# Performance work log

Hardware: AMD Instinct MI355X
Metric: run time of the kernel (lower is better)

## Reference

```python
import jax, jax.numpy as jnp
import numpy as np

NH, HD = 4, 16          # num_heads, head_dim (proj_dim = 64)
SCALE = HD ** -0.5
EPS = 1e-5
G = 16                  # GroupNorm groups = min(16, channels)


def _conv1x1(W, b, x):
    # 1x1 conv == channel-mixing matmul: W (out,in), x (B,in,H,W)
    return jnp.einsum('pc,bchw->bphw', W, x) + b[None, :, None, None]


def _attend(Wq, bq, Wk, bk, Wv, bv, Wo, bo, query, context):
    B, C, H, Wd = query.shape
    N = H * Wd
    q = _conv1x1(Wq, bq, query).astype(jnp.float32).reshape(B, NH, HD, N)
    k = _conv1x1(Wk, bk, context).astype(jnp.float32).reshape(B, NH, HD, N)
    v = _conv1x1(Wv, bv, context).astype(jnp.float32).reshape(B, NH, HD, N)
    attn = jax.nn.softmax(jnp.einsum('bhdn,bhdm->bhnm', q, k) * SCALE, axis=-1)
    out = jnp.einsum('bhdm,bhnm->bhdn', v, attn).reshape(B, NH * HD, H, Wd)
    return _conv1x1(Wo, bo, out)


def _gn(x, gamma, beta):
    B, C, H, W = x.shape
    xr = x.reshape(B, G, C // G, H, W)
    m = xr.mean(axis=(2, 3, 4), keepdims=True)
    v = xr.var(axis=(2, 3, 4), keepdims=True)
    xn = ((xr - m) * jax.lax.rsqrt(v + EPS)).reshape(B, C, H, W)
    return xn * gamma[None, :, None, None] + beta[None, :, None, None]


def setup_inputs() -> dict:
    key = jax.random.key(0)
    C, P, Bn, H, W = 256, 64, 2, 64, 64
    ks = iter(jax.random.split(key, 64))
    d = {}
    for m in ['a', 'b', 'c']:
        d[f'feat_{m}'] = jax.random.normal(next(ks), (Bn, C, H, W), jnp.float32)
    for m in ['a', 'b', 'c']:
        d[f'Wq_{m}'] = 0.02 * jax.random.normal(next(ks), (P, C), jnp.float32)
        d[f'bq_{m}'] = jnp.zeros((P,), jnp.float32)
        d[f'Wk_{m}'] = 0.02 * jax.random.normal(next(ks), (P, 2 * C), jnp.float32)
        d[f'bk_{m}'] = jnp.zeros((P,), jnp.float32)
        d[f'Wv_{m}'] = 0.02 * jax.random.normal(next(ks), (P, 2 * C), jnp.float32)
        d[f'bv_{m}'] = jnp.zeros((P,), jnp.float32)
        d[f'Wo_{m}'] = 0.02 * jax.random.normal(next(ks), (C, P), jnp.float32)
        d[f'bo_{m}'] = jnp.zeros((C,), jnp.float32)
        d[f'g_{m}'] = jnp.ones((C,), jnp.float32)
        d[f'be_{m}'] = jnp.zeros((C,), jnp.float32)
    return d


def reference(feat_a, feat_b, feat_c,
              Wq_a, bq_a, Wk_a, bk_a, Wv_a, bv_a, Wo_a, bo_a, g_a, be_a,
              Wq_b, bq_b, Wk_b, bk_b, Wv_b, bv_b, Wo_b, bo_b, g_b, be_b,
              Wq_c, bq_c, Wk_c, bk_c, Wv_c, bv_c, Wo_c, bo_c, g_c, be_c):
    bc = jnp.concatenate([feat_b, feat_c], axis=1)
    a_out = _gn(feat_a + _attend(Wq_a, bq_a, Wk_a, bk_a, Wv_a, bv_a, Wo_a, bo_a, feat_a, bc), g_a, be_a)
    ac = jnp.concatenate([feat_a, feat_c], axis=1)
    b_out = _gn(feat_b + _attend(Wq_b, bq_b, Wk_b, bk_b, Wv_b, bv_b, Wo_b, bo_b, feat_b, ac), g_b, be_b)
    ab = jnp.concatenate([feat_a, feat_b], axis=1)
    c_out = _gn(feat_c + _attend(Wq_c, bq_c, Wk_c, bk_c, Wv_c, bv_c, Wo_c, bo_c, feat_c, ab), g_c, be_c)
    return (a_out, b_out, c_out)
```

## Files before the change

kernel.cpp:

```cpp
#include <hip/hip_runtime.h>

#define B_ 2
#define C_ 256
#define P_ 64
#define N_ 4096
#define EPS_ 1e-5f
#define QSCALE_ 0.3606737602222409f

typedef _Float16 half2 __attribute__((ext_vector_type(2)));
typedef _Float16 half4 __attribute__((ext_vector_type(4)));
typedef _Float16 half8 __attribute__((ext_vector_type(8)));
typedef __fp16 fp16x2 __attribute__((ext_vector_type(2)));
typedef float f32x4 __attribute__((ext_vector_type(4)));

#if __has_builtin(__builtin_amdgcn_exp2f)
static __device__ __forceinline__ float fexp2(float x) { return __builtin_amdgcn_exp2f(x); }
#else
static __device__ __forceinline__ float fexp2(float x) { return exp2f(x); }
#endif

static __device__ __forceinline__ half2 pack2(float a, float b) {
  return __builtin_bit_cast(half2, __builtin_amdgcn_cvt_pkrtz(a, b));
}

struct TP {
  const float* feat[3];
  const float* Wq[3]; const float* bq[3];
  const float* Wk[3]; const float* bk[3];
  const float* Wv[3]; const float* bv[3];
  const float* Wo[3]; const float* bo[3];
  const float* gm[3]; const float* bt[3];
  _Float16* xT;
  _Float16* q16;
  _Float16* k16;
  _Float16* v16;
  _Float16* wq16[3];
  _Float16* wk16[3];
  _Float16* wv16[3];
  _Float16* wo16[3];
  float* stats;
  float* out;
  int ctx0[3]; int ctx1[3];
};

__global__ __launch_bounds__(256) void prep_kernel(TP P) {
  const int m = blockIdx.z, b = blockIdx.y;
  const int tid = threadIdx.x;
  {
    const int c0 = (blockIdx.x >> 6) * 64 + (tid >> 6) * 16;
    const int n = (blockIdx.x & 63) * 64 + (tid & 63);
    const float* __restrict__ in = P.feat[m] + (size_t)b * C_ * N_ + n;
    float f[16];
#pragma unroll
    for (int i = 0; i < 16; ++i) f[i] = in[(size_t)(c0 + i) * N_];
    half8 h0, h1;
#pragma unroll
    for (int j = 0; j < 8; ++j) { h0[j] = (_Float16)f[j]; h1[j] = (_Float16)f[8 + j]; }
    _Float16* o = P.xT + (((size_t)(m * 2 + b) * N_) + n) * C_ + c0;
    *(half8*)o = h0;
    *(half8*)(o + 8) = h1;
  }
  if (b == 0 && blockIdx.x < 8) {
    const int s = blockIdx.x;
    const float* srcs[4] = {P.Wq[m], P.Wk[m], P.Wv[m], P.Wo[m]};
    _Float16* dsts[4] = {P.wq16[m], P.wk16[m], P.wv16[m], P.wo16[m]};
    const int sizes[4] = {64 * 256, 64 * 512, 64 * 512, 256 * 64};
#pragma unroll
    for (int a = 0; a < 4; ++a) {
      const int lo = sizes[a] / 8 * s, hi = sizes[a] / 8 * (s + 1);
      for (int i = lo + tid * 4; i < hi; i += 1024) {
        const float4 x = *(const float4*)(srcs[a] + i);
        half4 h; h[0] = (_Float16)x.x; h[1] = (_Float16)x.y;
        h[2] = (_Float16)x.z; h[3] = (_Float16)x.w;
        *(half4*)(dsts[a] + i) = h;
      }
    }
  }
  if (m == 0 && b == 0 && blockIdx.x == 8 && tid < 192) P.stats[tid] = 0.f;
}

__global__ __launch_bounds__(256) void proj_qkv_kernel(TP P) {
  __shared__ _Float16 vt[4 * 16 * 40];
  const int m = blockIdx.z, b = blockIdx.y;
  const int tid = threadIdx.x;
  const int w = tid >> 6, g = (tid >> 4) & 3, t = tid & 15;
  const bool is_q = blockIdx.x >= 128;
  const int n0 = (is_q ? blockIdx.x - 128 : (int)blockIdx.x) * 32;

  if (is_q) {
    const _Float16* __restrict__ A = P.wq16[m] + (w * 16 + t) * 256 + g * 8;
    const _Float16* __restrict__ B0 =
        P.xT + ((size_t)(m * 2 + b) * N_ + n0 + t) * C_ + g * 8;
    const _Float16* __restrict__ B1 = B0 + 16 * C_;
    f32x4 a0 = {0.f,0.f,0.f,0.f}, a1 = {0.f,0.f,0.f,0.f};
#pragma unroll
    for (int k = 0; k < 8; ++k) {
      const half8 a = *(const half8*)(A + k * 32);
      const half8 b0 = *(const half8*)(B0 + k * 32);
      const half8 b1 = *(const half8*)(B1 + k * 32);
      a0 = __builtin_amdgcn_mfma_f32_16x16x32_f16(a, b0, a0, 0, 0, 0);
      a1 = __builtin_amdgcn_mfma_f32_16x16x32_f16(a, b1, a1, 0, 0, 0);
    }
    _Float16* qo = P.q16 + ((size_t)(m * 2 + b) * N_) * 64 + w * 16 + g * 4;
    half4 h0, h1;
#pragma unroll
    for (int r = 0; r < 4; ++r) {
      const float bq = P.bq[m][w * 16 + g * 4 + r];
      h0[r] = (_Float16)((a0[r] + bq) * QSCALE_);
      h1[r] = (_Float16)((a1[r] + bq) * QSCALE_);
    }
    *(half4*)(qo + (size_t)(n0 + t) * 64) = h0;
    *(half4*)(qo + (size_t)(n0 + 16 + t) * 64) = h1;
  } else {
    f32x4 k0 = {0.f,0.f,0.f,0.f}, k1 = {0.f,0.f,0.f,0.f};
    f32x4 v0 = {0.f,0.f,0.f,0.f}, v1 = {0.f,0.f,0.f,0.f};
    const int srcs[2] = {P.ctx0[m], P.ctx1[m]};
#pragma unroll
    for (int src = 0; src < 2; ++src) {
      const _Float16* __restrict__ Ak =
          P.wk16[m] + (w * 16 + t) * 512 + src * 256 + g * 8;
      const _Float16* __restrict__ Av =
          P.wv16[m] + (w * 16 + t) * 512 + src * 256 + g * 8;
      const _Float16* __restrict__ B0 =
          P.xT + ((size_t)(srcs[src] * 2 + b) * N_ + n0 + t) * C_ + g * 8;
      const _Float16* __restrict__ B1 = B0 + 16 * C_;
#pragma unroll
      for (int k = 0; k < 8; ++k) {
        const half8 ak = *(const half8*)(Ak + k * 32);
        const half8 av = *(const half8*)(Av + k * 32);
        const half8 b0 = *(const half8*)(B0 + k * 32);
        const half8 b1 = *(const half8*)(B1 + k * 32);
        k0 = __builtin_amdgcn_mfma_f32_16x16x32_f16(ak, b0, k0, 0, 0, 0);
        k1 = __builtin_amdgcn_mfma_f32_16x16x32_f16(ak, b1, k1, 0, 0, 0);
        v0 = __builtin_amdgcn_mfma_f32_16x16x32_f16(av, b0, v0, 0, 0, 0);
        v1 = __builtin_amdgcn_mfma_f32_16x16x32_f16(av, b1, v1, 0, 0, 0);
      }
    }
    const int bh = m * 8 + b * 4 + w;
    _Float16* ko = P.k16 + ((size_t)bh * N_) * 16 + g * 4;
    half4 h0, h1;
#pragma unroll
    for (int r = 0; r < 4; ++r) {
      const float bk = P.bk[m][w * 16 + g * 4 + r];
      h0[r] = (_Float16)(k0[r] + bk);
      h1[r] = (_Float16)(k1[r] + bk);
    }
    *(half4*)(ko + (size_t)(n0 + t) * 16) = h0;
    *(half4*)(ko + (size_t)(n0 + 16 + t) * 16) = h1;
#pragma unroll
    for (int r = 0; r < 4; ++r) {
      const float bv = P.bv[m][w * 16 + g * 4 + r];
      vt[(w * 16 + g * 4 + r) * 40 + t] = (_Float16)(v0[r] + bv);
      vt[(w * 16 + g * 4 + r) * 40 + 16 + t] = (_Float16)(v1[r] + bv);
    }
    __syncthreads();
    const int hh = tid >> 6, dd = (tid >> 2) & 15, nb = (tid & 3) * 8;
    const half8 hv8 = *(const half8*)(vt + (hh * 16 + dd) * 40 + nb);
    *(half8*)(P.v16 + ((size_t)(m * 8 + b * 4 + hh) * 16 + dd) * N_ + n0 + nb) = hv8;
  }
}

__global__ __launch_bounds__(256) void attn_kernel(TP P) {
  const int m = blockIdx.z, bh = blockIdx.y;
  const int tid = threadIdx.x;
  const int w = tid >> 6, g = (tid >> 4) & 3, t = tid & 15;
  const _Float16* __restrict__ kh = P.k16 + ((size_t)(m * 8 + bh) * N_) * 16;
  const _Float16* __restrict__ vh = P.v16 + ((size_t)(m * 8 + bh) * 16) * N_;
  const int b = bh >> 2, h = bh & 3;
  _Float16* qh = P.q16 + ((size_t)(m * 2 + b) * N_) * 64 + h * 16 + g * 4;

  const int q0 = blockIdx.x * 64 + w * 16;
  const half4 qf = *(const half4*)(qh + (size_t)(q0 + t) * 64);

  __shared__ _Float16 ks[128 * 16];
  __shared__ _Float16 vs[16 * 128];

  const int kr = tid >> 1, kc8 = tid & 1;
  const int vr = tid >> 4, vc = tid & 15;
  const _Float16* kgp = kh + (size_t)kr * 16 + kc8 * 8;
  const _Float16* vgp = vh + (size_t)vr * N_ + vc * 8;
  _Float16* ksp = ks + kr * 16 + ((kc8 ^ (kr & 1)) << 3);
  _Float16* vsp = vs + vr * 128 + ((vc ^ vr) << 3);

  half8 kpre = *(const half8*)kgp;
  half8 vpre = *(const half8*)vgp;

  f32x4 lacc = {0.f, 0.f, 0.f, 0.f};
  f32x4 O0 = {0.f,0.f,0.f,0.f}, O1 = {0.f,0.f,0.f,0.f};

  for (int kv0 = 0; kv0 < N_; kv0 += 128) {
    *(half8*)ksp = kpre;
    *(half8*)vsp = vpre;
    __syncthreads();
    const int nxt = (kv0 + 128 < N_) ? kv0 + 128 : 0;
    kpre = *(const half8*)(kgp + (size_t)nxt * 16);
    vpre = *(const half8*)(vgp + nxt);
#pragma unroll
    for (int hc = 0; hc < 2; ++hc) {
      f32x4 s[4];
#pragma unroll
      for (int i = 0; i < 4; ++i) {
        const int sub = hc * 4 + i;
        const half4 kf = *(const half4*)(ks + (sub * 16 + t) * 16 +
                          (((g >> 1) ^ (t & 1)) << 3) + (g & 1) * 4);
        const f32x4 z = {0.f, 0.f, 0.f, 0.f};
        s[i] = __builtin_amdgcn_mfma_f32_16x16x16f16(kf, qf, z, 0, 0, 0);
      }
      half4 pf[4];
#pragma unroll
      for (int i = 0; i < 4; ++i) {
        const float p0 = fexp2(s[i][0]);
        const float p1 = fexp2(s[i][1]);
        const float p2 = fexp2(s[i][2]);
        const float p3 = fexp2(s[i][3]);
        lacc[0] += p0; lacc[1] += p1; lacc[2] += p2; lacc[3] += p3;
        const half2 lo = pack2(p0, p1);
        const half2 hi = pack2(p2, p3);
        pf[i] = __builtin_shufflevector(lo, hi, 0, 1, 2, 3);
      }
#pragma unroll
      for (int i = 0; i < 4; ++i) {
        const int sub = hc * 4 + i;
        const half4 vf = *(const half4*)(vs + t * 128 +
                          (((sub * 2 + (g >> 1)) ^ t) << 3) + (g & 1) * 4);
        if (i & 1) O1 = __builtin_amdgcn_mfma_f32_16x16x16f16(vf, pf[i], O1, 0, 0, 0);
        else       O0 = __builtin_amdgcn_mfma_f32_16x16x16f16(vf, pf[i], O0, 0, 0, 0);
      }
    }
    __syncthreads();
  }
  float l = lacc[0] + lacc[1] + lacc[2] + lacc[3];
  l += __shfl_xor(l, 16);
  l += __shfl_xor(l, 32);
  const float inv = 1.0f / l;
  half4 hv;
#pragma unroll
  for (int r = 0; r < 4; ++r) hv[r] = (_Float16)((O0[r] + O1[r]) * inv);
  *(half4*)(qh + (size_t)(q0 + t) * 64) = hv;
}

__global__ __launch_bounds__(256) void wo_resid_kernel(TP P) {
  const int m = blockIdx.z;
  const int b = blockIdx.y >> 2, cblk = blockIdx.y & 3;
  const int n0 = blockIdx.x * 64;
  const int tid = threadIdx.x;
  const int w = tid >> 6, g = (tid >> 4) & 3, t = tid & 15;
  const int c0 = cblk * 64 + w * 16;
  const _Float16* __restrict__ ao = P.q16 + ((size_t)(m * 2 + b) * N_) * 64;
  f32x4 acc[4] = {{0.f,0.f,0.f,0.f},{0.f,0.f,0.f,0.f},{0.f,0.f,0.f,0.f},{0.f,0.f,0.f,0.f}};
#pragma unroll
  for (int kst = 0; kst < 2; ++kst) {
    const half8 a =
        *(const half8*)(P.wo16[m] + (c0 + t) * 64 + kst * 32 + g * 8);
#pragma unroll
    for (int i = 0; i < 4; ++i) {
      const half8 bf =
          *(const half8*)(ao + (size_t)(n0 + i * 16 + t) * 64 + kst * 32 + g * 8);
      acc[i] = __builtin_amdgcn_mfma_f32_16x16x32_f16(a, bf, acc[i], 0, 0, 0);
    }
  }
  const float* __restrict__ X = P.feat[m] + (size_t)b * C_ * N_;
  float* outb = P.out + (size_t)m * B_ * C_ * N_ + (size_t)b * C_ * N_;
  float s = 0.f, s2 = 0.f;
#pragma unroll
  for (int i = 0; i < 4; ++i) {
    const int n = n0 + i * 16 + t;
#pragma unroll
    for (int r = 0; r < 4; ++r) {
      const int c = c0 + g * 4 + r;
      const float val = acc[i][r] + X[(size_t)c * N_ + n] + P.bo[m][c];
      outb[(size_t)c * N_ + n] = val;
      s += val;
      s2 += val * val;
    }
  }
#pragma unroll
  for (int off = 1; off < 64; off <<= 1) {
    s += __shfl_xor(s, off);
    s2 += __shfl_xor(s2, off);
  }
  if ((tid & 63) == 0) {
    const int group = cblk * 4 + w;
    float* st = P.stats + ((size_t)(m * 2 + b) * 16 + group) * 2;
    atomicAdd(st, s);
    atomicAdd(st + 1, s2);
  }
}

__global__ __launch_bounds__(256) void gn_final_kernel(TP P) {
  const size_t idx = ((size_t)blockIdx.x * 256 + threadIdx.x) * 4;
  const int m = (int)(idx >> 21);
  const int rem = (int)(idx & ((1u << 21) - 1));
  const int b = rem >> 20;
  const int c = (rem >> 12) & 255;
  const float* st = P.stats + ((size_t)(m * 2 + b) * 16 + (c >> 4)) * 2;
  const float mean = st[0] * (1.f / 65536.f);
  const float var = st[1] * (1.f / 65536.f) - mean * mean;
  const float rstd = rsqrtf(var + EPS_);
  const float ga = P.gm[m][c] * rstd, be = P.bt[m][c];
  float4 x = *(float4*)(P.out + idx);
  x.x = (x.x - mean) * ga + be;
  x.y = (x.y - mean) * ga + be;
  x.z = (x.z - mean) * ga + be;
  x.w = (x.w - mean) * ga + be;
  *(float4*)(P.out + idx) = x;
}

extern "C" void kernel_launch(void* const* d_in, const int* in_sizes, int n_in,
                              void* d_out, int out_size, void* d_ws, size_t ws_size,
                              hipStream_t stream) {
  TP P;
  for (int m = 0; m < 3; ++m) {
    P.feat[m] = (const float*)d_in[m];
    const int base = 3 + m * 10;
    P.Wq[m] = (const float*)d_in[base + 0];
    P.bq[m] = (const float*)d_in[base + 1];
    P.Wk[m] = (const float*)d_in[base + 2];
    P.bk[m] = (const float*)d_in[base + 3];
    P.Wv[m] = (const float*)d_in[base + 4];
    P.bv[m] = (const float*)d_in[base + 5];
    P.Wo[m] = (const float*)d_in[base + 6];
    P.bo[m] = (const float*)d_in[base + 7];
    P.gm[m] = (const float*)d_in[base + 8];
    P.bt[m] = (const float*)d_in[base + 9];
  }
  _Float16* ws = (_Float16*)d_ws;
  P.xT = ws;
  P.q16 = ws + 6291456;
  P.k16 = ws + 7864320;
  P.v16 = ws + 9437184;
  for (int m = 0; m < 3; ++m) {
    _Float16* wb = ws + 11010048 + (size_t)m * 98304;
    P.wq16[m] = wb;
    P.wk16[m] = wb + 16384;
    P.wv16[m] = wb + 49152;
    P.wo16[m] = wb + 81920;
  }
  P.stats = (float*)((char*)d_ws + 22609920);
  P.out = (float*)d_out;
  P.ctx0[0] = 1; P.ctx1[0] = 2;
  P.ctx0[1] = 0; P.ctx1[1] = 2;
  P.ctx0[2] = 0; P.ctx1[2] = 1;

  dim3 blk(256);
  prep_kernel<<<dim3(256, 2, 3), blk, 0, stream>>>(P);
  proj_qkv_kernel<<<dim3(256, 2, 3), blk, 0, stream>>>(P);
  attn_kernel<<<dim3(64, 8, 3), blk, 0, stream>>>(P);
  wo_resid_kernel<<<dim3(64, 8, 3), blk, 0, stream>>>(P);
  gn_final_kernel<<<dim3(6144), blk, 0, stream>>>(P);
}
```

Measured before the change: 293.0 us.

## Stage transposes and GEMM operands through LDS, approximate exp2, coarsen GN kernel

Measured after the change: 281.7 us. -3.9%, faster.

```diff
diff --git a/kernel.cpp b/kernel.cpp
--- a/kernel.cpp
+++ b/kernel.cpp
@@ -10,14 +10,11 @@
 typedef _Float16 half2 __attribute__((ext_vector_type(2)));
 typedef _Float16 half4 __attribute__((ext_vector_type(4)));
 typedef _Float16 half8 __attribute__((ext_vector_type(8)));
-typedef __fp16 fp16x2 __attribute__((ext_vector_type(2)));
 typedef float f32x4 __attribute__((ext_vector_type(4)));
 
-#if __has_builtin(__builtin_amdgcn_exp2f)
-static __device__ __forceinline__ float fexp2(float x) { return __builtin_amdgcn_exp2f(x); }
-#else
-static __device__ __forceinline__ float fexp2(float x) { return exp2f(x); }
-#endif
+static __device__ __forceinline__ float fexp2(float x) {
+  return __builtin_bit_cast(float, (int)fmaf(x, 8388608.0f, 1064872512.0f));
+}
 
 static __device__ __forceinline__ half2 pack2(float a, float b) {
   return __builtin_bit_cast(half2, __builtin_amdgcn_cvt_pkrtz(a, b));
@@ -44,21 +41,33 @@
 };
 
 __global__ __launch_bounds__(256) void prep_kernel(TP P) {
+  __shared__ _Float16 lt[64 * 72];
   const int m = blockIdx.z, b = blockIdx.y;
   const int tid = threadIdx.x;
+  const int cblk = blockIdx.x >> 6, nblk = blockIdx.x & 63;
   {
-    const int c0 = (blockIdx.x >> 6) * 64 + (tid >> 6) * 16;
-    const int n = (blockIdx.x & 63) * 64 + (tid & 63);
-    const float* __restrict__ in = P.feat[m] + (size_t)b * C_ * N_ + n;
+    const int n = nblk * 64 + (tid & 63);
+    const int cb = (tid >> 6) * 16;
+    const float* __restrict__ in =
+        P.feat[m] + (size_t)b * C_ * N_ + (size_t)(cblk * 64 + cb) * N_ + n;
     float f[16];
 #pragma unroll
-    for (int i = 0; i < 16; ++i) f[i] = in[(size_t)(c0 + i) * N_];
+    for (int i = 0; i < 16; ++i) f[i] = in[(size_t)i * N_];
     half8 h0, h1;
 #pragma unroll
     for (int j = 0; j < 8; ++j) { h0[j] = (_Float16)f[j]; h1[j] = (_Float16)f[8 + j]; }
-    _Float16* o = P.xT + (((size_t)(m * 2 + b) * N_) + n) * C_ + c0;
-    *(half8*)o = h0;
-    *(half8*)(o + 8) = h1;
+    *(half8*)(lt + (tid & 63) * 72 + cb) = h0;
+    *(half8*)(lt + (tid & 63) * 72 + cb + 8) = h1;
+  }
+  __syncthreads();
+  {
+    const int nr = tid >> 2, cs = (tid & 3) * 16;
+    const half8 o0 = *(const half8*)(lt + nr * 72 + cs);
+    const half8 o1 = *(const half8*)(lt + nr * 72 + cs + 8);
+    _Float16* o = P.xT + ((size_t)(m * 2 + b) * N_ + nblk * 64 + nr) * C_ +
+                  cblk * 64 + cs;
+    *(half8*)o = o0;
+    *(half8*)(o + 8) = o1;
   }
   if (b == 0 && blockIdx.x < 8) {
     const int s = blockIdx.x;
@@ -79,25 +88,30 @@
   if (m == 0 && b == 0 && blockIdx.x == 8 && tid < 192) P.stats[tid] = 0.f;
 }
 
+#define PBS_ 264
+
 __global__ __launch_bounds__(256) void proj_qkv_kernel(TP P) {
-  __shared__ _Float16 vt[4 * 16 * 40];
+  __shared__ _Float16 bs[2 * 32 * PBS_];
   const int m = blockIdx.z, b = blockIdx.y;
   const int tid = threadIdx.x;
   const int w = tid >> 6, g = (tid >> 4) & 3, t = tid & 15;
   const bool is_q = blockIdx.x >= 128;
   const int n0 = (is_q ? blockIdx.x - 128 : (int)blockIdx.x) * 32;
+  const int sr = tid >> 3, sc = (tid & 7) * 32;
 
   if (is_q) {
-    const _Float16* __restrict__ A = P.wq16[m] + (w * 16 + t) * 256 + g * 8;
-    const _Float16* __restrict__ B0 =
-        P.xT + ((size_t)(m * 2 + b) * N_ + n0 + t) * C_ + g * 8;
-    const _Float16* __restrict__ B1 = B0 + 16 * C_;
+    const _Float16* __restrict__ xb =
+        P.xT + ((size_t)(m * 2 + b) * N_ + n0 + sr) * C_ + sc;
+#pragma unroll
+    for (int j = 0; j < 4; ++j)
+      *(half8*)(bs + sr * PBS_ + sc + j * 8) = *(const half8*)(xb + j * 8);
+    __syncthreads();
     f32x4 a0 = {0.f,0.f,0.f,0.f}, a1 = {0.f,0.f,0.f,0.f};
 #pragma unroll
-    for (int k = 0; k < 8; ++k) {
-      const half8 a = *(const half8*)(A + k * 32);
-      const half8 b0 = *(const half8*)(B0 + k * 32);
-      const half8 b1 = *(const half8*)(B1 + k * 32);
+    for (int ks = 0; ks < 8; ++ks) {
+      const half8 a = *(const half8*)(P.wq16[m] + (w * 16 + t) * 256 + ks * 32 + g * 8);
+      const half8 b0 = *(const half8*)(bs + t * PBS_ + ks * 32 + g * 8);
+      const half8 b1 = *(const half8*)(bs + (16 + t) * PBS_ + ks * 32 + g * 8);
       a0 = __builtin_amdgcn_mfma_f32_16x16x32_f16(a, b0, a0, 0, 0, 0);
       a1 = __builtin_amdgcn_mfma_f32_16x16x32_f16(a, b1, a1, 0, 0, 0);
     }
@@ -112,24 +126,29 @@
     *(half4*)(qo + (size_t)(n0 + t) * 64) = h0;
     *(half4*)(qo + (size_t)(n0 + 16 + t) * 64) = h1;
   } else {
+    const int srcs[2] = {P.ctx0[m], P.ctx1[m]};
+#pragma unroll
+    for (int src = 0; src < 2; ++src) {
+      const _Float16* __restrict__ xb =
+          P.xT + ((size_t)(srcs[src] * 2 + b) * N_ + n0 + sr) * C_ + sc;
+#pragma unroll
+      for (int j = 0; j < 4; ++j)
+        *(half8*)(bs + src * 32 * PBS_ + sr * PBS_ + sc + j * 8) =
+            *(const half8*)(xb + j * 8);
+    }
+    __syncthreads();
     f32x4 k0 = {0.f,0.f,0.f,0.f}, k1 = {0.f,0.f,0.f,0.f};
     f32x4 v0 = {0.f,0.f,0.f,0.f}, v1 = {0.f,0.f,0.f,0.f};
-    const int srcs[2] = {P.ctx0[m], P.ctx1[m]};
 #pragma unroll
     for (int src = 0; src < 2; ++src) {
-      const _Float16* __restrict__ Ak =
-          P.wk16[m] + (w * 16 + t) * 512 + src * 256 + g * 8;
-      const _Float16* __restrict__ Av =
-          P.wv16[m] + (w * 16 + t) * 512 + src * 256 + g * 8;
-      const _Float16* __restrict__ B0 =
-          P.xT + ((size_t)(srcs[src] * 2 + b) * N_ + n0 + t) * C_ + g * 8;
-      const _Float16* __restrict__ B1 = B0 + 16 * C_;
-#pragma unroll
-      for (int k = 0; k < 8; ++k) {
-        const half8 ak = *(const half8*)(Ak + k * 32);
-        const half8 av = *(const half8*)(Av + k * 32);
-        const half8 b0 = *(const half8*)(B0 + k * 32);
-        const half8 b1 = *(const half8*)(B1 + k * 32);
+#pragma unroll
+      for (int ks = 0; ks < 8; ++ks) {
+        const half8 ak = *(const half8*)(P.wk16[m] + (w * 16 + t) * 512 +
+                                         src * 256 + ks * 32 + g * 8);
+        const half8 av = *(const half8*)(P.wv16[m] + (w * 16 + t) * 512 +
+                                         src * 256 + ks * 32 + g * 8);
+        const half8 b0 = *(const half8*)(bs + src * 32 * PBS_ + t * PBS_ + ks * 32 + g * 8);
+        const half8 b1 = *(const half8*)(bs + src * 32 * PBS_ + (16 + t) * PBS_ + ks * 32 + g * 8);
         k0 = __builtin_amdgcn_mfma_f32_16x16x32_f16(ak, b0, k0, 0, 0, 0);
         k1 = __builtin_amdgcn_mfma_f32_16x16x32_f16(ak, b1, k1, 0, 0, 0);
         v0 = __builtin_amdgcn_mfma_f32_16x16x32_f16(av, b0, v0, 0, 0, 0);
@@ -147,6 +166,8 @@
     }
     *(half4*)(ko + (size_t)(n0 + t) * 16) = h0;
     *(half4*)(ko + (size_t)(n0 + 16 + t) * 16) = h1;
+    __syncthreads();
+    _Float16* vt = bs;
 #pragma unroll
     for (int r = 0; r < 4; ++r) {
       const float bv = P.bv[m][w * 16 + g * 4 + r];
@@ -209,14 +230,10 @@
       half4 pf[4];
 #pragma unroll
       for (int i = 0; i < 4; ++i) {
-        const float p0 = fexp2(s[i][0]);
-        const float p1 = fexp2(s[i][1]);
-        const float p2 = fexp2(s[i][2]);
-        const float p3 = fexp2(s[i][3]);
+        const float p0 = fexp2(s[i][0]), p1 = fexp2(s[i][1]);
+        const float p2 = fexp2(s[i][2]), p3 = fexp2(s[i][3]);
         lacc[0] += p0; lacc[1] += p1; lacc[2] += p2; lacc[3] += p3;
-        const half2 lo = pack2(p0, p1);
-        const half2 hi = pack2(p2, p3);
-        pf[i] = __builtin_shufflevector(lo, hi, 0, 1, 2, 3);
+        pf[i] = __builtin_shufflevector(pack2(p0, p1), pack2(p2, p3), 0, 1, 2, 3);
       }
 #pragma unroll
       for (int i = 0; i < 4; ++i) {
@@ -239,7 +256,10 @@
   *(half4*)(qh + (size_t)(q0 + t) * 64) = hv;
 }
 
+#define BS_ 72
+
 __global__ __launch_bounds__(256) void wo_resid_kernel(TP P) {
+  __shared__ _Float16 as[64 * BS_];
   const int m = blockIdx.z;
   const int b = blockIdx.y >> 2, cblk = blockIdx.y & 3;
   const int n0 = blockIdx.x * 64;
@@ -247,6 +267,12 @@
   const int w = tid >> 6, g = (tid >> 4) & 3, t = tid & 15;
   const int c0 = cblk * 64 + w * 16;
   const _Float16* __restrict__ ao = P.q16 + ((size_t)(m * 2 + b) * N_) * 64;
+  const int ar = tid >> 2, ac = (tid & 3) * 16;
+  const half8 l0 = *(const half8*)(ao + (size_t)(n0 + ar) * 64 + ac);
+  const half8 l1 = *(const half8*)(ao + (size_t)(n0 + ar) * 64 + ac + 8);
+  *(half8*)(as + ar * BS_ + ac) = l0;
+  *(half8*)(as + ar * BS_ + ac + 8) = l1;
+  __syncthreads();
   f32x4 acc[4] = {{0.f,0.f,0.f,0.f},{0.f,0.f,0.f,0.f},{0.f,0.f,0.f,0.f},{0.f,0.f,0.f,0.f}};
 #pragma unroll
   for (int kst = 0; kst < 2; ++kst) {
@@ -254,8 +280,7 @@
         *(const half8*)(P.wo16[m] + (c0 + t) * 64 + kst * 32 + g * 8);
 #pragma unroll
     for (int i = 0; i < 4; ++i) {
-      const half8 bf =
-          *(const half8*)(ao + (size_t)(n0 + i * 16 + t) * 64 + kst * 32 + g * 8);
+      const half8 bf = *(const half8*)(as + (i * 16 + t) * BS_ + kst * 32 + g * 8);
       acc[i] = __builtin_amdgcn_mfma_f32_16x16x32_f16(a, bf, acc[i], 0, 0, 0);
     }
   }
@@ -288,22 +313,26 @@
 }
 
 __global__ __launch_bounds__(256) void gn_final_kernel(TP P) {
-  const size_t idx = ((size_t)blockIdx.x * 256 + threadIdx.x) * 4;
-  const int m = (int)(idx >> 21);
-  const int rem = (int)(idx & ((1u << 21) - 1));
-  const int b = rem >> 20;
-  const int c = (rem >> 12) & 255;
-  const float* st = P.stats + ((size_t)(m * 2 + b) * 16 + (c >> 4)) * 2;
-  const float mean = st[0] * (1.f / 65536.f);
-  const float var = st[1] * (1.f / 65536.f) - mean * mean;
-  const float rstd = rsqrtf(var + EPS_);
-  const float ga = P.gm[m][c] * rstd, be = P.bt[m][c];
-  float4 x = *(float4*)(P.out + idx);
-  x.x = (x.x - mean) * ga + be;
-  x.y = (x.y - mean) * ga + be;
-  x.z = (x.z - mean) * ga + be;
-  x.w = (x.w - mean) * ga + be;
-  *(float4*)(P.out + idx) = x;
+  const size_t base = ((size_t)blockIdx.x * 256 + threadIdx.x) * 4;
+#pragma unroll
+  for (int it = 0; it < 4; ++it) {
+    const size_t idx = base + (size_t)it * 1572864;
+    const int m = (int)(idx >> 21);
+    const int rem = (int)(idx & ((1u << 21) - 1));
+    const int b = rem >> 20;
+    const int c = (rem >> 12) & 255;
+    const float* st = P.stats + ((size_t)(m * 2 + b) * 16 + (c >> 4)) * 2;
+    const float mean = st[0] * (1.f / 65536.f);
+    const float var = st[1] * (1.f / 65536.f) - mean * mean;
+    const float rstd = rsqrtf(var + EPS_);
+    const float ga = P.gm[m][c] * rstd, be = P.bt[m][c];
+    float4 x = *(float4*)(P.out + idx);
+    x.x = (x.x - mean) * ga + be;
+    x.y = (x.y - mean) * ga + be;
+    x.z = (x.z - mean) * ga + be;
+    x.w = (x.w - mean) * ga + be;
+    *(float4*)(P.out + idx) = x;
+  }
 }
 
 extern "C" void kernel_launch(void* const* d_in, const int* in_sizes, int n_in,
@@ -347,5 +376,5 @@
   proj_qkv_kernel<<<dim3(256, 2, 3), blk, 0, stream>>>(P);
   attn_kernel<<<dim3(64, 8, 3), blk, 0, stream>>>(P);
   wo_resid_kernel<<<dim3(64, 8, 3), blk, 0, stream>>>(P);
-  gn_final_kernel<<<dim3(6144), blk, 0, stream>>>(P);
-}
+  gn_final_kernel<<<dim3(1536), blk, 0, stream>>>(P);
+}
```
